# Kernel optimization log

Measured on AMD Instinct MI355X. Metric: run time of the kernel, lower is better.

Reference implementation:

```python
import jax, jax.numpy as jnp
import numpy as np

B, S, D = 16, 4096, 1024
NUM_DISEASES, NUM_STATES = 14, 2
THRESHOLD = 0.2


def setup_inputs() -> dict:
    key = jax.random.key(0)
    k1, k2 = jax.random.split(key)
    z_fused = jax.random.normal(k1, (B, S, D), dtype=jnp.float32)
    # xavier_uniform on M viewed as (num_diseases, num_states, d): fan per torch is
    # fan_in = num_states * d (last two dims flattened receptive field), fan_out = num_diseases... 
    # torch xavier on a 3D tensor: fan_in = D (last dim), fan_out = NUM_STATES, with receptive field = D.
    # Faithful enough init scale: limit = sqrt(6 / (fan_in + fan_out)).
    fan_in = NUM_STATES * D
    fan_out = NUM_DISEASES * D
    limit = float(np.sqrt(6.0 / (fan_in + fan_out)))
    M = jax.random.uniform(k2, (NUM_DISEASES, NUM_STATES, D), dtype=jnp.float32, minval=-limit, maxval=limit)
    return {"z_fused": z_fused, "M": M}


def reference(z_fused, M):
    d = z_fused.shape[-1]
    # mean pool over sequence -> [B, d]
    z_pooled = jnp.mean(z_fused, axis=1)
    # scores: [B, num_diseases, num_states]
    scores = jnp.einsum('bd,nsd->bns', z_pooled, M) / jnp.sqrt(jnp.asarray(d, z_fused.dtype))
    alpha = jax.nn.softmax(scores, axis=-1)
    mlc_probs = alpha[:, :, 1]                      # [B, num_diseases]
    alpha_hat = (mlc_probs > THRESHOLD).astype(z_fused.dtype)
    M_present = M[:, 1, :]                          # [num_diseases, d]
    R = alpha_hat @ M_present                       # [B, d]
    z_out = z_fused + R[:, None, :]                 # broadcast add over S
    return (z_out, mlc_probs)
```

## Files before the change

kernel.cpp:

```cpp
#include <hip/hip_runtime.h>
#include <math.h>

#define BB 16
#define SS 4096
#define DD 1024
#define ND 14
#define THRESH 0.2f

#define ADD_CH 128
#define AROWS (SS / ADD_CH)

typedef float vfloat4 __attribute__((ext_vector_type(4)));

__global__ __launch_bounds__(256) void pool_partial(
        const float4* __restrict__ z, float4* __restrict__ part, int rows) {
    const int b = blockIdx.x;
    const int c = blockIdx.y;
    const int t = threadIdx.x;
    const float4* p = z + ((size_t)b * SS + (size_t)c * rows) * (DD / 4) + t;
    float4 acc = {0.f, 0.f, 0.f, 0.f};
#pragma unroll 8
    for (int s = 0; s < rows; ++s) {
        float4 v = p[(size_t)s * (DD / 4)];
        acc.x += v.x; acc.y += v.y; acc.z += v.z; acc.w += v.w;
    }
    part[((size_t)b * gridDim.y + c) * (DD / 4) + t] = acc;
}

__global__ __launch_bounds__(256) void score_kernel(
        const float4* __restrict__ part, const float* __restrict__ M,
        float4* __restrict__ Rout, float* __restrict__ mlc_out, int chunks) {
    const int b = blockIdx.x;
    const int t = threadIdx.x;
    const int wave = t >> 6;
    const int lane = t & 63;

    __shared__ float pooled[DD];
    __shared__ float sc[ND * 2];
    __shared__ float hat[ND];

    float4 acc = {0.f, 0.f, 0.f, 0.f};
    const float4* p = part + (size_t)b * chunks * (DD / 4) + t;
    for (int c = 0; c < chunks; ++c) {
        float4 v = p[(size_t)c * (DD / 4)];
        acc.x += v.x; acc.y += v.y; acc.z += v.z; acc.w += v.w;
    }
    const float inv = 1.0f / (float)SS;
    ((float4*)pooled)[t] = make_float4(acc.x * inv, acc.y * inv,
                                       acc.z * inv, acc.w * inv);
    __syncthreads();

    for (int i = 0; i < 7; ++i) {
        const int idx = wave * 7 + i;
        const float* Mrow = M + (size_t)idx * DD;
        float partial = 0.f;
#pragma unroll
        for (int k = lane; k < DD; k += 64) partial += pooled[k] * Mrow[k];
        for (int off = 32; off > 0; off >>= 1)
            partial += __shfl_down(partial, off, 64);
        if (lane == 0) sc[idx] = partial * (1.0f / 32.0f);
    }
    __syncthreads();

    if (t < ND) {
        float a1 = 1.0f / (1.0f + expf(sc[2 * t] - sc[2 * t + 1]));
        mlc_out[b * ND + t] = a1;
        hat[t] = (a1 > THRESH) ? 1.0f : 0.0f;
    }
    __syncthreads();

    float4 r = {0.f, 0.f, 0.f, 0.f};
    const float4* M4 = (const float4*)M;
    for (int n = 0; n < ND; ++n) {
        if (hat[n] != 0.0f) {
            float4 m = M4[(size_t)(n * 2 + 1) * (DD / 4) + t];
            r.x += m.x; r.y += m.y; r.z += m.z; r.w += m.w;
        }
    }
    Rout[b * (DD / 4) + t] = r;
}

__global__ __launch_bounds__(256) void add_kernel(
        const vfloat4* __restrict__ z, const vfloat4* __restrict__ R,
        vfloat4* __restrict__ out) {
    const int b = blockIdx.x;
    const int c = blockIdx.y;
    const int t = threadIdx.x;
    const vfloat4 r = R[b * (DD / 4) + t];
    const size_t base = ((size_t)b * SS + (size_t)c * AROWS) * (DD / 4) + t;
#pragma unroll 8
    for (int s = 0; s < AROWS; ++s) {
        const size_t idx = base + (size_t)s * (DD / 4);
        vfloat4 v = __builtin_nontemporal_load(&z[idx]);
        v += r;
        __builtin_nontemporal_store(v, &out[idx]);
    }
}

extern "C" void kernel_launch(void* const* d_in, const int* in_sizes, int n_in,
                              void* d_out, int out_size, void* d_ws, size_t ws_size,
                              hipStream_t stream) {
    const float* z = (const float*)d_in[0];
    const float* M = (const float*)d_in[1];
    float* out = (float*)d_out;

    float* Rws = (float*)d_ws;
    float* part = Rws + (size_t)BB * DD;
    size_t avail = ws_size > (size_t)BB * DD * sizeof(float)
                       ? ws_size - (size_t)BB * DD * sizeof(float) : 0;
    int chunks = 128;
    while (chunks > 1 && (size_t)BB * chunks * DD * sizeof(float) > avail)
        chunks >>= 1;
    if (chunks < 1) chunks = 1;
    const int rows = SS / chunks;

    pool_partial<<<dim3(BB, chunks), 256, 0, stream>>>(
        (const float4*)z, (float4*)part, rows);
    score_kernel<<<BB, 256, 0, stream>>>(
        (const float4*)part, M, (float4*)Rws,
        out + (size_t)BB * SS * DD, chunks);
    add_kernel<<<dim3(BB, ADD_CH), 256, 0, stream>>>(
        (const vfloat4*)z, (const vfloat4*)Rws, (vfloat4*)out);
}
```

Measured before the change: 551.6 us.

## Fuse pooling, scoring and broadcast add into one cooperative kernel with grid sync

Replaces the three-launch pipeline with a single cooperative kernel. Each block pools its chunk of rows, a grid-wide sync follows, then every block recomputes the scores and R redundantly and adds R to the same rows it just read. The intent is to remove launch gaps and hope the second read of z hits the large last-level cache. The cost is a grid barrier, redundant per-block score work, and reliance on 1024 blocks being co-resident. The fallback add kernel also switches from nontemporal to normal loads.

```diff
diff --git a/kernel.cpp b/kernel.cpp
--- a/kernel.cpp
+++ b/kernel.cpp
@@ -1,5 +1,8 @@
 #include <hip/hip_runtime.h>
+#include <hip/hip_cooperative_groups.h>
 #include <math.h>
+
+namespace cg = cooperative_groups;
 
 #define BB 16
 #define SS 4096
@@ -7,10 +10,88 @@
 #define ND 14
 #define THRESH 0.2f
 
-#define ADD_CH 128
-#define AROWS (SS / ADD_CH)
+#define CPB 64
+#define ROWS (SS / CPB)
+#define GRID (BB * CPB)
 
 typedef float vfloat4 __attribute__((ext_vector_type(4)));
+
+__global__ __launch_bounds__(256, 4) void fused_kernel(
+        const float4* __restrict__ z, float4* __restrict__ part,
+        vfloat4* __restrict__ out, float* __restrict__ mlc_out,
+        const float* __restrict__ M) {
+    const int blk = blockIdx.x;
+    const int b = blk >> 6;
+    const int c = blk & (CPB - 1);
+    const int t = threadIdx.x;
+    const int wave = t >> 6;
+    const int lane = t & 63;
+
+    const float4* zp = z + ((size_t)b * SS + (size_t)c * ROWS) * (DD / 4) + t;
+    float4 acc = {0.f, 0.f, 0.f, 0.f};
+#pragma unroll 8
+    for (int s = 0; s < ROWS; ++s) {
+        float4 v = zp[(size_t)s * (DD / 4)];
+        acc.x += v.x; acc.y += v.y; acc.z += v.z; acc.w += v.w;
+    }
+    part[((size_t)b * CPB + c) * (DD / 4) + t] = acc;
+
+    cg::this_grid().sync();
+
+    __shared__ float pooled[DD];
+    __shared__ float sc[ND * 2];
+    __shared__ float hat[ND];
+
+    float4 racc = {0.f, 0.f, 0.f, 0.f};
+    const float4* pp = part + (size_t)b * CPB * (DD / 4) + t;
+    for (int cc = 0; cc < CPB; ++cc) {
+        float4 v = pp[(size_t)cc * (DD / 4)];
+        racc.x += v.x; racc.y += v.y; racc.z += v.z; racc.w += v.w;
+    }
+    const float inv = 1.0f / (float)SS;
+    ((float4*)pooled)[t] = make_float4(racc.x * inv, racc.y * inv,
+                                       racc.z * inv, racc.w * inv);
+    __syncthreads();
+
+    for (int i = 0; i < 7; ++i) {
+        const int idx = wave * 7 + i;
+        const float* Mrow = M + (size_t)idx * DD;
+        float p = 0.f;
+#pragma unroll
+        for (int k = lane; k < DD; k += 64) p += pooled[k] * Mrow[k];
+        for (int off = 32; off > 0; off >>= 1)
+            p += __shfl_down(p, off, 64);
+        if (lane == 0) sc[idx] = p * (1.0f / 32.0f);
+    }
+    __syncthreads();
+
+    if (t < ND) {
+        float a1 = 1.0f / (1.0f + expf(sc[2 * t] - sc[2 * t + 1]));
+        if (c == 0) mlc_out[b * ND + t] = a1;
+        hat[t] = (a1 > THRESH) ? 1.0f : 0.0f;
+    }
+    __syncthreads();
+
+    float4 r = {0.f, 0.f, 0.f, 0.f};
+    const float4* M4 = (const float4*)M;
+    for (int n = 0; n < ND; ++n) {
+        if (hat[n] != 0.0f) {
+            float4 m = M4[(size_t)(n * 2 + 1) * (DD / 4) + t];
+            r.x += m.x; r.y += m.y; r.z += m.z; r.w += m.w;
+        }
+    }
+    vfloat4 rv; rv.x = r.x; rv.y = r.y; rv.z = r.z; rv.w = r.w;
+
+    const vfloat4* zz = (const vfloat4*)z;
+    const size_t base = ((size_t)b * SS + (size_t)c * ROWS) * (DD / 4) + t;
+#pragma unroll 8
+    for (int s = 0; s < ROWS; ++s) {
+        const size_t idx = base + (size_t)s * (DD / 4);
+        vfloat4 v = zz[idx];
+        v += rv;
+        __builtin_nontemporal_store(v, &out[idx]);
+    }
+}
 
 __global__ __launch_bounds__(256) void pool_partial(
         const float4* __restrict__ z, float4* __restrict__ part, int rows) {
@@ -87,11 +168,11 @@
     const int c = blockIdx.y;
     const int t = threadIdx.x;
     const vfloat4 r = R[b * (DD / 4) + t];
-    const size_t base = ((size_t)b * SS + (size_t)c * AROWS) * (DD / 4) + t;
-#pragma unroll 8
-    for (int s = 0; s < AROWS; ++s) {
+    const size_t base = ((size_t)b * SS + (size_t)c * 32) * (DD / 4) + t;
+#pragma unroll 8
+    for (int s = 0; s < 32; ++s) {
         const size_t idx = base + (size_t)s * (DD / 4);
-        vfloat4 v = __builtin_nontemporal_load(&z[idx]);
+        vfloat4 v = z[idx];
         v += r;
         __builtin_nontemporal_store(v, &out[idx]);
     }
@@ -106,6 +187,21 @@
 
     float* Rws = (float*)d_ws;
     float* part = Rws + (size_t)BB * DD;
+
+    const size_t need_fused = ((size_t)BB * DD + (size_t)BB * CPB * DD) * sizeof(float);
+
+    if (ws_size >= need_fused) {
+        const float4* z4 = (const float4*)z;
+        float4* part4 = (float4*)part;
+        vfloat4* out4 = (vfloat4*)out;
+        float* mlc = out + (size_t)BB * SS * DD;
+        void* args[] = {(void*)&z4, (void*)&part4, (void*)&out4,
+                        (void*)&mlc, (void*)&M};
+        hipError_t err = hipLaunchCooperativeKernel(
+            (const void*)fused_kernel, dim3(GRID), dim3(256), args, 0, stream);
+        if (err == hipSuccess) return;
+    }
+
     size_t avail = ws_size > (size_t)BB * DD * sizeof(float)
                        ? ws_size - (size_t)BB * DD * sizeof(float) : 0;
     int chunks = 128;
@@ -119,6 +215,6 @@
     score_kernel<<<BB, 256, 0, stream>>>(
         (const float4*)part, M, (float4*)Rws,
         out + (size_t)BB * SS * DD, chunks);
-    add_kernel<<<dim3(BB, ADD_CH), 256, 0, stream>>>(
+    add_kernel<<<dim3(BB, SS / 32), 256, 0, stream>>>(
         (const vfloat4*)z, (const vfloat4*)Rws, (vfloat4*)out);
 }
```

New measurement: 645.2 us. 1.17x slower.
